# Performance work log

Measured on AMD Instinct MI355X. Metric: run time of the kernel, lower is better.

The kernel has to match this reference:

```python
import jax, jax.numpy as jnp
from jax import lax
import numpy as np

BS = 16          # batch (must be even, K % BS == 0)
K = 8192         # MoCo queue size
H = 768          # hidden size
G = 5            # rank_num (number of GMM components)
UPDATE_MEAN = 0.1


def _norm(x):
    return x / jnp.linalg.norm(x, axis=-1, keepdims=True)


def setup_inputs() -> dict:
    key = jax.random.key(0)
    ks = jax.random.split(key, 6)
    sent_q = _norm(jax.random.normal(ks[0], (BS, H), jnp.float32))
    sent_k = _norm(jax.random.normal(ks[1], (BS, H), jnp.float32))
    queue = _norm(jax.random.normal(ks[2], (K, H), jnp.float32))
    mu = jax.random.normal(ks[3], (G, H), jnp.float32)
    lg_sigma2 = jax.random.normal(ks[4], (G, H), jnp.float32)
    pi = jnp.ones((G,), jnp.float32)
    rank_mean = jax.random.uniform(ks[5], (G,), jnp.float32)
    return {"sent_q": sent_q, "sent_k": sent_k, "queue": queue,
            "mu": mu, "lg_sigma2": lg_sigma2, "pi": pi, "rank_mean": rank_mean}


def gaussian_mixture(features, mu, lg_sigma2, pi):
    # features: [B, N, H]; mu/lg_sigma2: [G, H]; pi: [G]
    # expo_{bng} = sum_h (f_{bnh} - mu_{gh})^2 / sigma2_{gh}, expanded so we never
    # materialize the [B, N, G, H] diff tensor the torch code builds.
    inv = jnp.exp(-lg_sigma2)                                   # [G, H]
    expo = (jnp.einsum('bnh,gh->bng', features * features, inv)
            - 2.0 * jnp.einsum('bnh,gh->bng', features, mu * inv)
            + jnp.sum(mu * mu * inv, axis=-1))                  # [B, N, G]
    lg2piD = features.shape[-1] * np.log(2.0 * np.pi).astype(np.float32)
    l_prob = -0.5 * (lg2piD + jnp.sum(lg_sigma2, axis=-1) + expo)
    logits = jax.nn.log_softmax(pi) + l_prob
    logits_norm = logits - jnp.max(logits, axis=-1, keepdims=True)
    prob = jax.nn.softmax(logits_norm, axis=-1)
    return logits_norm, prob


def reference(sent_q, sent_k, queue, mu, lg_sigma2, pi, rank_mean):
    bs = sent_q.shape[0]
    all_feature = jnp.concatenate([sent_k, queue], axis=0)       # [N, H]
    N = all_feature.shape[0]

    # golden mask (is_pair=True): pair j of i is (i + bs//2) mod bs
    pair_label = jnp.concatenate([jnp.arange(bs)[bs // 2:], jnp.arange(bs)[:bs // 2]])
    golden = jnp.arange(bs)[:, None] == pair_label[None, :]      # [bs, bs]
    golden_mask = jnp.concatenate(
        [golden, jnp.zeros((bs, N - bs), bool)], axis=1)         # [bs, N]

    sample_sim = sent_q @ all_feature.T                          # [bs, N]

    # map_scores_to_ranks (rank_mean detached)
    rm = lax.stop_gradient(rank_mean)
    cts_pred = jnp.argmin(jnp.abs(sample_sim[..., None] - rm[None, None, :]), axis=-1)
    cts_dist = jnp.floor((sample_sim + 1.0) / 2.0 * G).astype(jnp.int32)

    # GMM on detached broadcast diff [bs, N, H]
    f = lax.stop_gradient(sent_q)[:, None, :] - lax.stop_gradient(all_feature)[None, :, :]
    gmm_logits, gmm_prob = gaussian_mixture(f, mu, lg_sigma2, pi)
    gmm_pred = jnp.argmax(gmm_prob, axis=-1)                     # [bs, N]

    eye = jnp.arange(bs)[:, None] == jnp.arange(N)[None, :]      # [bs, N]
    # torch: gmm_label aliases cts_pred and is masked_fill_'d in place
    gmm_label = jnp.where(eye | golden_mask, G - 1, cts_pred)

    # update_rank_mean(sample_sim, gmm_pred) -- uses gmm_pred BEFORE cts_label masking
    oh = jax.nn.one_hot(gmm_pred, G, dtype=sample_sim.dtype)     # [bs, N, G]
    counts = jnp.sum(oh, axis=(0, 1))                            # [G]
    sums = jnp.einsum('bng,bn->g', oh, sample_sim)
    cur_rank_mean = sums / (counts + 1e-12)
    upd = (counts != 0).astype(rank_mean.dtype)
    new_rank_mean = (1.0 - upd * UPDATE_MEAN) * rank_mean + upd * UPDATE_MEAN * cur_rank_mean

    # torch: cts_label aliases gmm_pred and masked_fill_ mutates both in place;
    # the returned 'gmm pred' therefore equals this masked version.
    cts_label = jnp.where(golden_mask, G - 1, gmm_pred)

    logits_max = lax.stop_gradient(jnp.max(sample_sim, axis=1, keepdims=True))
    cts_logits = sample_sim - logits_max

    # acc pred: zero the (i, i) entries (torch scatter of 0 at col i)
    acc_pred = sample_sim * (1.0 - eye.astype(sample_sim.dtype))

    return (gmm_logits, gmm_prob, cts_logits, acc_pred, new_rank_mean,
            gmm_label, cts_label, cts_dist)


if __name__ == "__main__":
    outs = reference(**setup_inputs())
    for o in outs:
        print(o.shape, o.dtype)
```

## Files before the change

kernel.cpp:

```cpp
#include <hip/hip_runtime.h>
#include <stdint.h>

#define BS 16
#define KQ 8192
#define NTOT (BS + KQ)
#define H 768
#define G 5
#define UPD 0.1f
#define FPAD 772
#define ROWS 8
#define LG2PID (768.0f * 1.8378770664093453f)

#define SZ_BN   (BS*NTOT)
#define SZ_BNG  (BS*NTOT*G)
#define O_GLOGITS 0
#define O_GPROB   (SZ_BNG)
#define O_CTSLOG  (2*SZ_BNG)
#define O_ACC     (O_CTSLOG + SZ_BN)
#define O_NRM     (O_ACC + SZ_BN)
#define O_GLABEL  (O_NRM + G)
#define O_CLABEL  (O_GLABEL + SZ_BN)
#define O_CDIST   (O_CLABEL + SZ_BN)

#define W_INV   0
#define W_MSC   (G*H)
#define W_BB    (2*G*H)
#define W_CNT8  (W_BB + BS*G)
#define W_SUM8  (W_CNT8 + 128)
#define W_RMX8  (W_SUM8 + 128)
#define W_DIAG  (W_RMX8 + 128)
#define W_QP    (W_DIAG + BS)

__device__ __forceinline__ unsigned enc_f(float f) {
    unsigned u = __float_as_uint(f);
    return (u & 0x80000000u) ? ~u : (u | 0x80000000u);
}
__device__ __forceinline__ float dec_f(unsigned k) {
    return (k & 0x80000000u) ? __uint_as_float(k & 0x7fffffffu) : __uint_as_float(~k);
}

__device__ __forceinline__ float wave_red_sum(float v) {
    #pragma unroll
    for (int off = 32; off > 0; off >>= 1) v += __shfl_down(v, off, 64);
    return v;
}

__device__ __forceinline__ void gload_lds16(const float* g, float* l) {
    __builtin_amdgcn_global_load_lds(
        (const __attribute__((address_space(1))) void*)(g),
        (__attribute__((address_space(3))) void*)(l), 16, 0, 0);
}

__global__ __launch_bounds__(256) void prep_kernel(
    const float* __restrict__ sent_q, const float* __restrict__ mu,
    const float* __restrict__ lg,     const float* __restrict__ pi,
    float* __restrict__ ws)
{
    const int t = threadIdx.x;
    const int lane = t & 63;
    const int w = t >> 6;
    const int bx = blockIdx.x;

    if (bx < 20) {
        const int task = bx * 4 + w;
        const int b = task / G, g = task % G;
        float accP = 0.f, accU = 0.f, accC = 0.f, accS = 0.f;
        for (int h = lane; h < H; h += 64) {
            float qv  = sent_q[b*H + h];
            float lgv = lg[g*H + h];
            float m   = mu[g*H + h];
            float iv  = expf(-lgv);
            accP = fmaf(qv*qv, iv, accP);
            accU = fmaf(qv*m,  iv, accU);
            accC = fmaf(m*m,   iv, accC);
            accS += lgv;
        }
        accP = wave_red_sum(accP);
        accU = wave_red_sum(accU);
        accC = wave_red_sum(accC);
        accS = wave_red_sum(accS);
        if (lane == 0) {
            float mx = pi[0];
            #pragma unroll
            for (int gg = 1; gg < G; ++gg) mx = fmaxf(mx, pi[gg]);
            float s = 0.f;
            #pragma unroll
            for (int gg = 0; gg < G; ++gg) s += expf(pi[gg] - mx);
            float lse = mx + logf(s);
            ws[W_BB + task] =
                (pi[g] - lse) - 0.5f*(LG2PID + accS + accC + accP - 2.f*accU);
        }
    } else if (bx < 35) {
        const int i = (bx - 20) * 256 + t;
        float iv = expf(-lg[i]);
        ws[W_INV + i] = iv;
        ws[W_MSC + i] = mu[i] * iv;
    } else if (bx == 35) {
        for (int i = t; i < 384; i += 256) ws[W_CNT8 + i] = 0.f;
    } else {
        const int gid = (bx - 36) * 256 + t;
        const int i = gid >> 4, b = gid & 15;
        float4 v = *reinterpret_cast<const float4*>(sent_q + b*H + i*4);
        reinterpret_cast<float4*>(ws + W_QP)[gid] = v;
    }
}

__global__ __launch_bounds__(512, 4) void main_kernel(
    const float* __restrict__ sent_k,
    const float* __restrict__ queue,
    const float* __restrict__ rank_mean,
    const float* __restrict__ invp,
    const float* __restrict__ mscp,
    const float* __restrict__ BBp,
    const float* __restrict__ qpp,
    float* cnt8, float* sum8, unsigned* rmx8, float* diagp,
    float* __restrict__ out)
{
    __shared__ __align__(16) float fbuf[ROWS * FPAD];
    __shared__ float red[2][64][21];
    __shared__ float s_BB[BS*G];
    __shared__ float s_A2[ROWS*G];
    __shared__ float s_cnt[G], s_sum[G];

    const int t    = threadIdx.x;
    const int lane = t & 63;
    const int w    = t >> 6;
    const int s    = t >> 8;
    const int wq   = w & 3;
    const int b    = lane >> 2;
    const int nl   = lane & 3;
    const int row  = s*4 + nl;
    const int bx   = blockIdx.x;
    const int n    = bx * ROWS + row;

    if (t < BS*G) s_BB[t] = BBp[t];
    if (t >= 128 && t < 128 + G) { s_cnt[t-128] = 0.f; s_sum[t-128] = 0.f; }

    {
        const int rn = bx * ROWS + w;
        const float* src = ((rn < BS) ? (sent_k + rn*H) : (queue + (rn - BS)*H)) + lane*4;
        #pragma unroll
        for (int k = 0; k < 3; ++k)
            gload_lds16(src + k*256, &fbuf[w*FPAD + k*256]);
    }
    __syncthreads();

    {
        const float* frow = fbuf + w*FPAD;
        float Tp[G] = {0.f,0.f,0.f,0.f,0.f};
        float Vp[G] = {0.f,0.f,0.f,0.f,0.f};
        #pragma unroll 1
        for (int j = 0; j < 3; ++j) {
            const int h = j*256 + lane*4;
            const float4 fv = *reinterpret_cast<const float4*>(frow + h);
            const float fx2 = fv.x*fv.x, fy2 = fv.y*fv.y, fz2 = fv.z*fv.z, fw2 = fv.w*fv.w;
            #pragma unroll
            for (int g = 0; g < G; ++g) {
                const float4 iv = *reinterpret_cast<const float4*>(invp + g*H + h);
                const float4 mv = *reinterpret_cast<const float4*>(mscp + g*H + h);
                Tp[g] = fmaf(fx2, iv.x, Tp[g]);
                Tp[g] = fmaf(fy2, iv.y, Tp[g]);
                Tp[g] = fmaf(fz2, iv.z, Tp[g]);
                Tp[g] = fmaf(fw2, iv.w, Tp[g]);
                Vp[g] = fmaf(fv.x, mv.x, Vp[g]);
                Vp[g] = fmaf(fv.y, mv.y, Vp[g]);
                Vp[g] = fmaf(fv.z, mv.z, Vp[g]);
                Vp[g] = fmaf(fv.w, mv.w, Vp[g]);
            }
        }
        #pragma unroll
        for (int g = 0; g < G; ++g) {
            float T = wave_red_sum(Tp[g]);
            float V = wave_red_sum(Vp[g]);
            if (lane == 0) s_A2[w*G + g] = 0.5f*T + V;
        }
    }

    const int hu = __builtin_amdgcn_readfirstlane(wq * 192);
    const float4* q4 = reinterpret_cast<const float4*>(qpp) + (hu >> 2) * 16 + b;
    const float* fb = fbuf + row*FPAD + hu;
    float sim = 0.f;
    float R[G] = {0.f, 0.f, 0.f, 0.f, 0.f};
    #pragma unroll 4
    for (int i = 0; i < 48; ++i) {
        const float4 qv = q4[i * 16];
        const float4 fv = *reinterpret_cast<const float4*>(fb + i*4);
        float p0 = qv.x * fv.x;
        float p1 = qv.y * fv.y;
        float p2 = qv.z * fv.z;
        float p3 = qv.w * fv.w;
        sim += (p0 + p1) + (p2 + p3);
        #pragma unroll
        for (int g = 0; g < G; ++g) {
            const float* iv = invp + g*H + hu + i*4;
            R[g] = fmaf(p3, iv[3], fmaf(p2, iv[2], fmaf(p1, iv[1], fmaf(p0, iv[0], R[g]))));
        }
    }

    if (wq) {
        red[s][lane][(wq-1)*6 + 0] = sim;
        #pragma unroll
        for (int g = 0; g < G; ++g) red[s][lane][(wq-1)*6 + 1 + g] = R[g];
    }
    __syncthreads();

    if (wq == 0) {
        #pragma unroll
        for (int qq = 0; qq < 3; ++qq) {
            sim += red[s][lane][qq*6];
            #pragma unroll
            for (int g = 0; g < G; ++g) R[g] += red[s][lane][qq*6 + 1 + g];
        }

        float lgt[G];
        #pragma unroll
        for (int g = 0; g < G; ++g)
            lgt[g] = s_BB[b*G + g] - s_A2[row*G + g] + R[g];
        float mx = lgt[0];
        #pragma unroll
        for (int g = 1; g < G; ++g) mx = fmaxf(mx, lgt[g]);

        const int bn = b * NTOT + n;
        float e[G], se = 0.f;
        #pragma unroll
        for (int g = 0; g < G; ++g) {
            float ln = lgt[g] - mx;
            out[O_GLOGITS + (size_t)bn * G + g] = ln;
            e[g] = expf(ln);
            se += e[g];
        }
        int pred = 0; float bestp = -1.f;
        #pragma unroll
        for (int g = 0; g < G; ++g) {
            float pg = e[g] / se;
            out[O_GPROB + (size_t)bn * G + g] = pg;
            if (pg > bestp) { bestp = pg; pred = g; }
        }

        int cp = 0; float bd = fabsf(sim - rank_mean[0]);
        #pragma unroll
        for (int g = 1; g < G; ++g) {
            float d = fabsf(sim - rank_mean[g]);
            if (d < bd) { bd = d; cp = g; }
        }

        float cdist = floorf((sim + 1.0f) * 0.5f * (float)G);

        bool eyev = (n == b);
        bool gold = (n < BS) && (n == ((b + BS/2) & (BS - 1)));

        out[O_GLABEL + bn] = (eyev || gold) ? (float)(G - 1) : (float)cp;
        out[O_CLABEL + bn] = gold ? (float)(G - 1) : (float)pred;
        out[O_ACC    + bn] = eyev ? 0.f : sim;
        out[O_CDIST  + bn] = cdist;
        if (eyev) diagp[b] = sim;

        atomicAdd(&s_cnt[pred], 1.f);
        atomicAdd(&s_sum[pred], sim);

        float m4 = sim;
        m4 = fmaxf(m4, __shfl_down(m4, 2, 4));
        m4 = fmaxf(m4, __shfl_down(m4, 1, 4));
        if (nl == 0) atomicMax(&rmx8[(bx & 7) * 16 + b], enc_f(m4));
    }
    __syncthreads();
    if (t < G) {
        atomicAdd(&cnt8[(bx & 7) * 16 + t], s_cnt[t]);
        atomicAdd(&sum8[(bx & 7) * 16 + t], s_sum[t]);
    }
}

__global__ __launch_bounds__(256) void final_kernel(
    const float* __restrict__ rank_mean,
    const float* __restrict__ cnt8, const float* __restrict__ sum8,
    const unsigned* __restrict__ rmx8, const float* __restrict__ diagp,
    float* __restrict__ out)
{
    const int i4 = blockIdx.x * 256 + threadIdx.x;
    if (i4 < G) {
        float c = 0.f, s = 0.f;
        #pragma unroll
        for (int j = 0; j < 8; ++j) { c += cnt8[j*16 + i4]; s += sum8[j*16 + i4]; }
        float cur = s / (c + 1e-12f);
        float u = (c != 0.f) ? 1.f : 0.f;
        out[O_NRM + i4] = (1.f - u * UPD) * rank_mean[i4] + u * UPD * cur;
    }
    if (i4 >= SZ_BN/4) return;
    const int i0 = i4 * 4;
    const int b  = i0 / NTOT;
    const int n0 = i0 - b * NTOT;
    unsigned mk = 0u;
    #pragma unroll
    for (int j = 0; j < 8; ++j) mk = max(mk, rmx8[j*16 + b]);
    const float rm = dec_f(mk);
    float4 v = *reinterpret_cast<const float4*>(&out[O_ACC + i0]);
    if (b >= n0 && b < n0 + 4) {
        float d = diagp[b];
        int r = b - n0;
        if (r == 0) v.x = d; else if (r == 1) v.y = d;
        else if (r == 2) v.z = d; else v.w = d;
    }
    float4 o;
    o.x = v.x - rm; o.y = v.y - rm; o.z = v.z - rm; o.w = v.w - rm;
    *reinterpret_cast<float4*>(&out[O_CTSLOG + i0]) = o;
}

extern "C" void kernel_launch(void* const* d_in, const int* in_sizes, int n_in,
                              void* d_out, int out_size, void* d_ws, size_t ws_size,
                              hipStream_t stream) {
    const float* sent_q    = (const float*)d_in[0];
    const float* sent_k    = (const float*)d_in[1];
    const float* queue     = (const float*)d_in[2];
    const float* mu        = (const float*)d_in[3];
    const float* lg        = (const float*)d_in[4];
    const float* pi        = (const float*)d_in[5];
    const float* rank_mean = (const float*)d_in[6];
    float* out = (float*)d_out;
    float* ws  = (float*)d_ws;

    prep_kernel<<<48, 256, 0, stream>>>(sent_q, mu, lg, pi, ws);

    main_kernel<<<NTOT / ROWS, 512, 0, stream>>>(
        sent_k, queue, rank_mean,
        ws + W_INV, ws + W_MSC, ws + W_BB, ws + W_QP,
        ws + W_CNT8, ws + W_SUM8,
        reinterpret_cast<unsigned*>(ws + W_RMX8), ws + W_DIAG,
        out);

    final_kernel<<<(SZ_BN/4 + 255) / 256, 256, 0, stream>>>(
        rank_mean, ws + W_CNT8, ws + W_SUM8,
        reinterpret_cast<const unsigned*>(ws + W_RMX8), ws + W_DIAG,
        out);
}
```

Measured before the change: 124.7 us.

## Process three rows per lane in main kernel to reuse query and inv-sigma loads

Each block now handles 12 feature rows with 256 threads (4 waves), and every lane computes three rows at once. The query float4 and the inv-sigma values are loaded once and reused across three rows, which cuts global/L1 load traffic per FMA, and the cross-wave reduction is reshaped to match. The cost is more registers per thread, lower launch bounds, a smaller grid with fewer blocks, and more serial per-lane epilogue work.

```diff
diff --git a/kernel.cpp b/kernel.cpp
--- a/kernel.cpp
+++ b/kernel.cpp
@@ -8,7 +8,8 @@
 #define G 5
 #define UPD 0.1f
 #define FPAD 772
-#define ROWS 8
+#define ROWS 12
+#define RPL 3
 #define LG2PID (768.0f * 1.8378770664093453f)
 
 #define SZ_BN   (BS*NTOT)
@@ -105,7 +106,7 @@
     }
 }
 
-__global__ __launch_bounds__(512, 4) void main_kernel(
+__global__ __launch_bounds__(256, 2) void main_kernel(
     const float* __restrict__ sent_k,
     const float* __restrict__ queue,
     const float* __restrict__ rank_mean,
@@ -117,7 +118,7 @@
     float* __restrict__ out)
 {
     __shared__ __align__(16) float fbuf[ROWS * FPAD];
-    __shared__ float red[2][64][21];
+    __shared__ float red[3][64][19];
     __shared__ float s_BB[BS*G];
     __shared__ float s_A2[ROWS*G];
     __shared__ float s_cnt[G], s_sum[G];
@@ -125,28 +126,30 @@
     const int t    = threadIdx.x;
     const int lane = t & 63;
     const int w    = t >> 6;
-    const int s    = t >> 8;
-    const int wq   = w & 3;
     const int b    = lane >> 2;
-    const int nl   = lane & 3;
-    const int row  = s*4 + nl;
+    const int nl0  = lane & 3;
     const int bx   = blockIdx.x;
-    const int n    = bx * ROWS + row;
 
     if (t < BS*G) s_BB[t] = BBp[t];
     if (t >= 128 && t < 128 + G) { s_cnt[t-128] = 0.f; s_sum[t-128] = 0.f; }
 
     {
-        const int rn = bx * ROWS + w;
-        const float* src = ((rn < BS) ? (sent_k + rn*H) : (queue + (rn - BS)*H)) + lane*4;
-        #pragma unroll
-        for (int k = 0; k < 3; ++k)
-            gload_lds16(src + k*256, &fbuf[w*FPAD + k*256]);
+        #pragma unroll
+        for (int rr = 0; rr < 3; ++rr) {
+            const int r = 3*w + rr;
+            const int rn = bx * ROWS + r;
+            const float* src = ((rn < BS) ? (sent_k + rn*H) : (queue + (rn - BS)*H)) + lane*4;
+            #pragma unroll
+            for (int k = 0; k < 3; ++k)
+                gload_lds16(src + k*256, &fbuf[r*FPAD + k*256]);
+        }
     }
     __syncthreads();
 
-    {
-        const float* frow = fbuf + w*FPAD;
+    #pragma unroll 1
+    for (int rr = 0; rr < 3; ++rr) {
+        const int r = 3*w + rr;
+        const float* frow = fbuf + r*FPAD;
         float Tp[G] = {0.f,0.f,0.f,0.f,0.f};
         float Vp[G] = {0.f,0.f,0.f,0.f,0.f};
         #pragma unroll 1
@@ -172,96 +175,119 @@
         for (int g = 0; g < G; ++g) {
             float T = wave_red_sum(Tp[g]);
             float V = wave_red_sum(Vp[g]);
-            if (lane == 0) s_A2[w*G + g] = 0.5f*T + V;
-        }
-    }
-
-    const int hu = __builtin_amdgcn_readfirstlane(wq * 192);
+            if (lane == 0) s_A2[r*G + g] = 0.5f*T + V;
+        }
+    }
+
+    const int hu = __builtin_amdgcn_readfirstlane(w * 192);
     const float4* q4 = reinterpret_cast<const float4*>(qpp) + (hu >> 2) * 16 + b;
-    const float* fb = fbuf + row*FPAD + hu;
-    float sim = 0.f;
-    float R[G] = {0.f, 0.f, 0.f, 0.f, 0.f};
+    const float* fb0 = fbuf + (nl0    )*FPAD + hu;
+    const float* fb1 = fbuf + (nl0 + 4)*FPAD + hu;
+    const float* fb2 = fbuf + (nl0 + 8)*FPAD + hu;
+    float sim0 = 0.f, sim1 = 0.f, sim2 = 0.f;
+    float R[RPL][G] = {};
     #pragma unroll 4
     for (int i = 0; i < 48; ++i) {
         const float4 qv = q4[i * 16];
-        const float4 fv = *reinterpret_cast<const float4*>(fb + i*4);
-        float p0 = qv.x * fv.x;
-        float p1 = qv.y * fv.y;
-        float p2 = qv.z * fv.z;
-        float p3 = qv.w * fv.w;
-        sim += (p0 + p1) + (p2 + p3);
+        const float4 f0 = *reinterpret_cast<const float4*>(fb0 + i*4);
+        const float4 f1 = *reinterpret_cast<const float4*>(fb1 + i*4);
+        const float4 f2 = *reinterpret_cast<const float4*>(fb2 + i*4);
+        float a0 = qv.x*f0.x, a1 = qv.y*f0.y, a2 = qv.z*f0.z, a3 = qv.w*f0.w;
+        float b0 = qv.x*f1.x, b1 = qv.y*f1.y, b2 = qv.z*f1.z, b3 = qv.w*f1.w;
+        float c0 = qv.x*f2.x, c1 = qv.y*f2.y, c2 = qv.z*f2.z, c3 = qv.w*f2.w;
+        sim0 += (a0 + a1) + (a2 + a3);
+        sim1 += (b0 + b1) + (b2 + b3);
+        sim2 += (c0 + c1) + (c2 + c3);
         #pragma unroll
         for (int g = 0; g < G; ++g) {
             const float* iv = invp + g*H + hu + i*4;
-            R[g] = fmaf(p3, iv[3], fmaf(p2, iv[2], fmaf(p1, iv[1], fmaf(p0, iv[0], R[g]))));
-        }
-    }
-
-    if (wq) {
-        red[s][lane][(wq-1)*6 + 0] = sim;
-        #pragma unroll
-        for (int g = 0; g < G; ++g) red[s][lane][(wq-1)*6 + 1 + g] = R[g];
+            const float i0 = iv[0], i1 = iv[1], i2 = iv[2], i3 = iv[3];
+            R[0][g] = fmaf(a3, i3, fmaf(a2, i2, fmaf(a1, i1, fmaf(a0, i0, R[0][g]))));
+            R[1][g] = fmaf(b3, i3, fmaf(b2, i2, fmaf(b1, i1, fmaf(b0, i0, R[1][g]))));
+            R[2][g] = fmaf(c3, i3, fmaf(c2, i2, fmaf(c1, i1, fmaf(c0, i0, R[2][g]))));
+        }
+    }
+    float sim[RPL] = {sim0, sim1, sim2};
+
+    if (w) {
+        #pragma unroll
+        for (int r = 0; r < RPL; ++r) {
+            red[w-1][lane][r*6 + 0] = sim[r];
+            #pragma unroll
+            for (int g = 0; g < G; ++g) red[w-1][lane][r*6 + 1 + g] = R[r][g];
+        }
     }
     __syncthreads();
 
-    if (wq == 0) {
+    if (w == 0) {
         #pragma unroll
         for (int qq = 0; qq < 3; ++qq) {
-            sim += red[s][lane][qq*6];
-            #pragma unroll
-            for (int g = 0; g < G; ++g) R[g] += red[s][lane][qq*6 + 1 + g];
-        }
-
-        float lgt[G];
-        #pragma unroll
-        for (int g = 0; g < G; ++g)
-            lgt[g] = s_BB[b*G + g] - s_A2[row*G + g] + R[g];
-        float mx = lgt[0];
-        #pragma unroll
-        for (int g = 1; g < G; ++g) mx = fmaxf(mx, lgt[g]);
-
-        const int bn = b * NTOT + n;
-        float e[G], se = 0.f;
-        #pragma unroll
-        for (int g = 0; g < G; ++g) {
-            float ln = lgt[g] - mx;
-            out[O_GLOGITS + (size_t)bn * G + g] = ln;
-            e[g] = expf(ln);
-            se += e[g];
-        }
-        int pred = 0; float bestp = -1.f;
-        #pragma unroll
-        for (int g = 0; g < G; ++g) {
-            float pg = e[g] / se;
-            out[O_GPROB + (size_t)bn * G + g] = pg;
-            if (pg > bestp) { bestp = pg; pred = g; }
-        }
-
-        int cp = 0; float bd = fabsf(sim - rank_mean[0]);
-        #pragma unroll
-        for (int g = 1; g < G; ++g) {
-            float d = fabsf(sim - rank_mean[g]);
-            if (d < bd) { bd = d; cp = g; }
-        }
-
-        float cdist = floorf((sim + 1.0f) * 0.5f * (float)G);
-
-        bool eyev = (n == b);
-        bool gold = (n < BS) && (n == ((b + BS/2) & (BS - 1)));
-
-        out[O_GLABEL + bn] = (eyev || gold) ? (float)(G - 1) : (float)cp;
-        out[O_CLABEL + bn] = gold ? (float)(G - 1) : (float)pred;
-        out[O_ACC    + bn] = eyev ? 0.f : sim;
-        out[O_CDIST  + bn] = cdist;
-        if (eyev) diagp[b] = sim;
-
-        atomicAdd(&s_cnt[pred], 1.f);
-        atomicAdd(&s_sum[pred], sim);
-
-        float m4 = sim;
-        m4 = fmaxf(m4, __shfl_down(m4, 2, 4));
-        m4 = fmaxf(m4, __shfl_down(m4, 1, 4));
-        if (nl == 0) atomicMax(&rmx8[(bx & 7) * 16 + b], enc_f(m4));
+            #pragma unroll
+            for (int r = 0; r < RPL; ++r) {
+                sim[r] += red[qq][lane][r*6];
+                #pragma unroll
+                for (int g = 0; g < G; ++g) R[r][g] += red[qq][lane][r*6 + 1 + g];
+            }
+        }
+
+        float m3 = -1e30f;
+        #pragma unroll
+        for (int r = 0; r < RPL; ++r) {
+            const int row = nl0 + r*4;
+            const int n   = bx * ROWS + row;
+
+            float lgt[G];
+            #pragma unroll
+            for (int g = 0; g < G; ++g)
+                lgt[g] = s_BB[b*G + g] - s_A2[row*G + g] + R[r][g];
+            float mx = lgt[0];
+            #pragma unroll
+            for (int g = 1; g < G; ++g) mx = fmaxf(mx, lgt[g]);
+
+            const int bn = b * NTOT + n;
+            float e[G], se = 0.f;
+            #pragma unroll
+            for (int g = 0; g < G; ++g) {
+                float ln = lgt[g] - mx;
+                out[O_GLOGITS + (size_t)bn * G + g] = ln;
+                e[g] = expf(ln);
+                se += e[g];
+            }
+            int pred = 0; float bestp = -1.f;
+            #pragma unroll
+            for (int g = 0; g < G; ++g) {
+                float pg = e[g] / se;
+                out[O_GPROB + (size_t)bn * G + g] = pg;
+                if (pg > bestp) { bestp = pg; pred = g; }
+            }
+
+            int cp = 0; float bd = fabsf(sim[r] - rank_mean[0]);
+            #pragma unroll
+            for (int g = 1; g < G; ++g) {
+                float d = fabsf(sim[r] - rank_mean[g]);
+                if (d < bd) { bd = d; cp = g; }
+            }
+
+            float cdist = floorf((sim[r] + 1.0f) * 0.5f * (float)G);
+
+            bool eyev = (n == b);
+            bool gold = (n < BS) && (n == ((b + BS/2) & (BS - 1)));
+
+            out[O_GLABEL + bn] = (eyev || gold) ? (float)(G - 1) : (float)cp;
+            out[O_CLABEL + bn] = gold ? (float)(G - 1) : (float)pred;
+            out[O_ACC    + bn] = eyev ? 0.f : sim[r];
+            out[O_CDIST  + bn] = cdist;
+            if (eyev) diagp[b] = sim[r];
+
+            atomicAdd(&s_cnt[pred], 1.f);
+            atomicAdd(&s_sum[pred], sim[r]);
+
+            m3 = fmaxf(m3, sim[r]);
+        }
+
+        m3 = fmaxf(m3, __shfl_down(m3, 2, 4));
+        m3 = fmaxf(m3, __shfl_down(m3, 1, 4));
+        if (nl0 == 0) atomicMax(&rmx8[(bx & 7) * 16 + b], enc_f(m3));
     }
     __syncthreads();
     if (t < G) {
@@ -320,7 +346,7 @@
 
     prep_kernel<<<48, 256, 0, stream>>>(sent_q, mu, lg, pi, ws);
 
-    main_kernel<<<NTOT / ROWS, 512, 0, stream>>>(
+    main_kernel<<<NTOT / ROWS, 256, 0, stream>>>(
         sent_k, queue, rank_mean,
         ws + W_INV, ws + W_MSC, ws + W_BB, ws + W_QP,
         ws + W_CNT8, ws + W_SUM8,
```

After: 126.8 us. Within noise of the previous version (+1.7%).
